# Optimization experiments

Measured on AMD Instinct MI355X. Metric: run time of the kernel, lower is better.

## Reference

```python
import jax, jax.numpy as jnp
import numpy as np

B, C, H, W = 4, 512, 128, 128
CQK = C // 8


def setup_inputs() -> dict:
    key = jax.random.key(0)
    ks = jax.random.split(key, 4)
    def w(k, shape, fan_in):
        return jax.random.normal(k, shape, jnp.float32) * np.float32(1.0 / np.sqrt(fan_in))
    return {
        "x": jax.random.normal(ks[0], (B, C, H, W), jnp.float32),
        "Wq": w(ks[1], (CQK, C), C), "bq": jnp.zeros((CQK,), jnp.float32),
        "Wk": w(ks[2], (CQK, C), C), "bk": jnp.zeros((CQK,), jnp.float32),
        "Wv": w(ks[3], (C, C), C), "bv": jnp.zeros((C,), jnp.float32),
    }


def _criss_cross(q, k, v):
    # q,k: [B, Cqk, H, W]; v: [B, C, H, W]
    _, _, h, w = q.shape
    # row energies: query at (y,x) vs keys (y, i) for all i -> [B, W(i), H, W]
    e_row = jnp.einsum('bchw,bchi->bihw', q, k)
    # column energies incl. self: query at (y,x) vs keys (j, x) -> [B, H(j), H, W]
    e_col = jnp.einsum('bchw,bcjw->bjhw', q, k)
    # CCNet's ca_weight excludes j == y from the column part (self term is
    # already counted once in the row part at i == x). Mask it to -inf so the
    # softmax matches the [B, H+W-1, H, W] energy exactly (masked weight = 0).
    diag = jnp.eye(h, dtype=bool)[None, :, :, None]  # [1, H(j), H(y), 1]
    e_col = jnp.where(diag, -jnp.inf, e_col)
    attn = jax.nn.softmax(jnp.concatenate([e_row, e_col], axis=1), axis=1)
    a_row, a_col = attn[:, :w], attn[:, w:]
    # ca_map: aggregate values along the same row and same column
    out = (jnp.einsum('bihw,bchi->bchw', a_row, v)
           + jnp.einsum('bjhw,bcjw->bchw', a_col, v))
    return out


def reference(x, Wq, bq, Wk, bk, Wv, bv):
    # 1x1 convs == per-pixel channel matmuls
    proj = lambda Wm, bm: jnp.einsum('bchw,oc->bohw', x, Wm) + bm[None, :, None, None]
    q = proj(Wq, bq)
    k = proj(Wk, bk)
    v = proj(Wv, bv)
    return _criss_cross(q, k, v)
```

## Files before the change

kernel.cpp:

```cpp
#include <hip/hip_runtime.h>
#include <hip/hip_bf16.h>

namespace {
constexpr int kB = 4;
constexpr int kC = 512;
constexpr int kH = 128;
constexpr int kW = 128;
constexpr int kCQK = 64;
constexpr int kL = kH * kW;
constexpr int kO = 640;

constexpr size_t OFF_WALL = 0;
constexpr size_t OFF_BALL = (size_t)kO * kC;
constexpr size_t OFF_QKV  = OFF_BALL + kO;
constexpr size_t OFF_E    = OFF_QKV + (size_t)kB * kO * kL;
constexpr size_t WS_FLOATS = OFF_E + (size_t)kB * kH * kW * 256;

typedef __attribute__((ext_vector_type(8))) short bf16x8;
typedef __attribute__((ext_vector_type(4))) float f32x4;

__device__ __forceinline__ unsigned short f32_to_bf16_rn(float f) {
  unsigned u = __float_as_uint(f);
  unsigned r = (u + 0x7FFFu + ((u >> 16) & 1u)) >> 16;
  return (unsigned short)r;
}
__device__ __forceinline__ float bf16_to_f32(unsigned short h) {
  return __uint_as_float(((unsigned)h) << 16);
}
__device__ __forceinline__ unsigned pack_bf16x2(float a, float b) {
  return (unsigned)f32_to_bf16_rn(a) | ((unsigned)f32_to_bf16_rn(b) << 16);
}
constexpr int SOW = 17;
constexpr int SOC = 16 * SOW + 1;
constexpr int ROW_SW = 132;
constexpr size_t AROWT_OFF = 2097152;
constexpr size_t QH_OFF = 0;
constexpr size_t QL_OFF = 1048576;
constexpr size_t KH_OFF = 2097152;
constexpr size_t KL_OFF = 3145728;
constexpr size_t CTMP_OFF = 8388608;
constexpr int VT_SC = 68;
constexpr int VT_SW = 16 * VT_SC + 4;
constexpr size_t VFRAG_B = (size_t)kW * 32 * 4 * 64 * 8;
}

__global__ __launch_bounds__(256) void pack_w(
    const float* __restrict__ Wq, const float* __restrict__ bq,
    const float* __restrict__ Wk, const float* __restrict__ bk,
    const float* __restrict__ Wv, const float* __restrict__ bv,
    short* __restrict__ wpk, float* __restrict__ ball) {
  const int r = blockIdx.x;
  const int t = threadIdx.x;
  const float* src;
  if (r < 64) {
    src = Wq + (size_t)r * kC;
    if (t == 0) ball[r] = bq[r];
  } else if (r < 128) {
    src = Wk + (size_t)(r - 64) * kC;
    if (t == 0) ball[r] = bk[r - 64];
  } else {
    src = Wv + (size_t)(r - 128) * kC;
    if (t == 0) ball[r] = bv[r - 128];
  }
#pragma unroll
  for (int p = 0; p < 2; ++p) {
    const int c = p * 256 + t;
    const float v = src[c];
    const unsigned short h = f32_to_bf16_rn(v);
    const unsigned short l = f32_to_bf16_rn(v - bf16_to_f32(h));
    wpk[(size_t)r * kC + c] = (short)h;
    wpk[(size_t)kO * kC + (size_t)r * kC + c] = (short)l;
  }
}

__global__ __launch_bounds__(256) void pack_x(
    const float* __restrict__ x, short* __restrict__ xpk, int b) {
  __shared__ float sT[64][65];
  const int l0 = blockIdx.x * 64;
  const int c0 = blockIdx.y * 64;
  const int t = threadIdx.x;
  const float* xb = x + (size_t)b * kC * kL;
#pragma unroll
  for (int p = 0; p < 4; ++p) {
    const int ch = p * 256 + t;
    const int c = ch >> 4, l4 = (ch & 15) * 4;
    float4 v = *(const float4*)(xb + (size_t)(c0 + c) * kL + l0 + l4);
    sT[c][l4 + 0] = v.x; sT[c][l4 + 1] = v.y; sT[c][l4 + 2] = v.z; sT[c][l4 + 3] = v.w;
  }
  __syncthreads();
#pragma unroll
  for (int p = 0; p < 2; ++p) {
    const int ch = p * 256 + t;
    const int l = ch >> 3, cg = ch & 7;
    short hi[8], lo[8];
#pragma unroll
    for (int j = 0; j < 8; ++j) {
      const float v = sT[cg * 8 + j][l];
      const unsigned short h = f32_to_bf16_rn(v);
      hi[j] = (short)h;
      lo[j] = (short)f32_to_bf16_rn(v - bf16_to_f32(h));
    }
    short* dh = xpk + (size_t)(l0 + l) * kC + c0 + cg * 8;
    *(bf16x8*)dh = *(bf16x8*)hi;
    *(bf16x8*)(dh + (size_t)kL * kC) = *(bf16x8*)lo;
  }
}

__global__ __launch_bounds__(256, 2) void proj_mfma(
    const short* __restrict__ xpk, const short* __restrict__ wpk,
    const float* __restrict__ ball, float* __restrict__ qkv, int b) {
  __shared__ short A_h[128 * 64];
  __shared__ short A_l[128 * 64];
  __shared__ short B_h[128 * 64];
  __shared__ short B_l[128 * 64];
  const int mt = blockIdx.x;
  const int n0 = blockIdx.y * 128;
  const int m0 = mt * 128;
  const bool qk = (mt == 0);
  const int t = threadIdx.x;
  const int wid = t >> 6, lane = t & 63;
  const int wr = wid >> 1, wc = wid & 1;
  const int lr = lane & 15, lg = lane >> 4;
  const int srow8 = lane >> 3;
  const int skg = (lane & 7) ^ srow8;

  f32x4 acc[4][4];
#pragma unroll
  for (int i = 0; i < 4; ++i)
#pragma unroll
    for (int j = 0; j < 4; ++j) acc[i][j] = (f32x4)(0.f);

  for (int kt = 0; kt < 8; ++kt) {
    const int k0 = kt * 64;
#pragma unroll
    for (int p = 0; p < 4; ++p) {
      const int ck = p * 4 + wid;
      const int row = ck * 8 + srow8;
      const short* srcA = wpk + (size_t)(m0 + row) * kC + k0 + skg * 8;
      const short* srcB = xpk + (size_t)(n0 + row) * kC + k0 + skg * 8;
      __builtin_amdgcn_global_load_lds(
          (const __attribute__((address_space(1))) void*)srcA,
          (__attribute__((address_space(3))) void*)&A_h[ck * 512], 16, 0, 0);
      __builtin_amdgcn_global_load_lds(
          (const __attribute__((address_space(1))) void*)(srcA + (size_t)kO * kC),
          (__attribute__((address_space(3))) void*)&A_l[ck * 512], 16, 0, 0);
      __builtin_amdgcn_global_load_lds(
          (const __attribute__((address_space(1))) void*)srcB,
          (__attribute__((address_space(3))) void*)&B_h[ck * 512], 16, 0, 0);
      if (qk)
        __builtin_amdgcn_global_load_lds(
            (const __attribute__((address_space(1))) void*)(srcB + (size_t)kL * kC),
            (__attribute__((address_space(3))) void*)&B_l[ck * 512], 16, 0, 0);
    }
    __syncthreads();
#pragma unroll
    for (int ks = 0; ks < 2; ++ks) {
      bf16x8 ah[4], al[4], bh[4], bl[4];
#pragma unroll
      for (int mf = 0; mf < 4; ++mf) {
        const int row = wr * 64 + mf * 16 + lr;
        const int kg = ks * 4 + lg;
        const int off = row * 64 + ((kg ^ (row & 7)) << 3);
        ah[mf] = *(const bf16x8*)&A_h[off];
        al[mf] = *(const bf16x8*)&A_l[off];
      }
#pragma unroll
      for (int nf = 0; nf < 4; ++nf) {
        const int row = wc * 64 + nf * 16 + lr;
        const int kg = ks * 4 + lg;
        const int off = row * 64 + ((kg ^ (row & 7)) << 3);
        bh[nf] = *(const bf16x8*)&B_h[off];
        if (qk) bl[nf] = *(const bf16x8*)&B_l[off];
      }
#pragma unroll
      for (int mf = 0; mf < 4; ++mf)
#pragma unroll
        for (int nf = 0; nf < 4; ++nf) {
          acc[mf][nf] = __builtin_amdgcn_mfma_f32_16x16x32_bf16(
              ah[mf], bh[nf], acc[mf][nf], 0, 0, 0);
          acc[mf][nf] = __builtin_amdgcn_mfma_f32_16x16x32_bf16(
              al[mf], bh[nf], acc[mf][nf], 0, 0, 0);
          if (qk)
            acc[mf][nf] = __builtin_amdgcn_mfma_f32_16x16x32_bf16(
                ah[mf], bl[nf], acc[mf][nf], 0, 0, 0);
        }
    }
    __syncthreads();
  }
  if (qk) {
    unsigned short* qw = (unsigned short*)qkv + (size_t)b * kO * kL * 2
        + (wr ? KH_OFF : QH_OFF);
#pragma unroll
    for (int mf = 0; mf < 4; ++mf) {
      const int c0 = mf * 16 + lg * 4;
#pragma unroll
      for (int nf = 0; nf < 4; ++nf) {
        const int l = n0 + wc * 64 + nf * 16 + lr;
        unsigned short hi4[4], lo4[4];
#pragma unroll
        for (int r = 0; r < 4; ++r) {
          const float val = acc[mf][nf][r] + ball[wr * 64 + c0 + r];
          const unsigned short h = f32_to_bf16_rn(val);
          hi4[r] = h;
          lo4[r] = f32_to_bf16_rn(val - bf16_to_f32(h));
        }
        unsigned short* d = qw + ((size_t)l * 64 + c0);
        *(uint2*)d = *(uint2*)hi4;
        *(uint2*)(d + QL_OFF) = *(uint2*)lo4;
      }
    }
  } else {
    unsigned short* vbf =
        (unsigned short*)(qkv + ((size_t)b * kO + 128) * kL);
#pragma unroll
    for (int mf = 0; mf < 4; ++mf) {
#pragma unroll
      for (int r = 0; r < 4; ++r) {
        const int m = m0 + wr * 64 + mf * 16 + lg * 4 + r;
        const float bias = ball[m];
        unsigned short* dst = vbf + (size_t)(m - 128) * kL + n0 + wc * 64;
#pragma unroll
        for (int nf = 0; nf < 4; ++nf) {
          dst[nf * 16 + lr] = f32_to_bf16_rn(acc[mf][nf][r] + bias);
        }
      }
    }
  }
}

template <int COL>
__global__ __launch_bounds__(256) void escore_mfma(
    const float* qkv, float* __restrict__ e) {
  const int bi = blockIdx.x;
  const int b = bi >> 7, idx = bi & 127;
  const int t = threadIdx.x;
  const int wid = t >> 6, lane = t & 63;
  const int wj = wid >> 1, wh = wid & 1;
  const int lr = lane & 15, lg = lane >> 4;

  const unsigned short* qkb = (const unsigned short*)qkv + (size_t)b * kO * kL * 2;
  const size_t baseoff = COL ? (size_t)idx * 64 : (size_t)idx * 8192;
  const int rstride = COL ? 8192 : 64;

  f32x4 acc[4][4];
#pragma unroll
  for (int i = 0; i < 4; ++i)
#pragma unroll
    for (int j = 0; j < 4; ++j) acc[i][j] = (f32x4)(0.f);

#pragma unroll
  for (int ks = 0; ks < 2; ++ks) {
    bf16x8 ah[4], al[4], bh[4], bl[4];
#pragma unroll
    for (int mf = 0; mf < 4; ++mf) {
      const size_t ro = baseoff + (size_t)(wj * 64 + mf * 16 + lr) * rstride
          + ks * 32 + lg * 8;
      ah[mf] = *(const bf16x8*)(qkb + KH_OFF + ro);
      al[mf] = *(const bf16x8*)(qkb + KL_OFF + ro);
    }
#pragma unroll
    for (int nf = 0; nf < 4; ++nf) {
      const size_t ro = baseoff + (size_t)(wh * 64 + nf * 16 + lr) * rstride
          + ks * 32 + lg * 8;
      bh[nf] = *(const bf16x8*)(qkb + QH_OFF + ro);
      bl[nf] = *(const bf16x8*)(qkb + QL_OFF + ro);
    }
#pragma unroll
    for (int mf = 0; mf < 4; ++mf)
#pragma unroll
      for (int nf = 0; nf < 4; ++nf) {
        acc[mf][nf] = __builtin_amdgcn_mfma_f32_16x16x32_bf16(
            ah[mf], bh[nf], acc[mf][nf], 0, 0, 0);
        acc[mf][nf] = __builtin_amdgcn_mfma_f32_16x16x32_bf16(
            ah[mf], bl[nf], acc[mf][nf], 0, 0, 0);
        acc[mf][nf] = __builtin_amdgcn_mfma_f32_16x16x32_bf16(
            al[mf], bh[nf], acc[mf][nf], 0, 0, 0);
      }
  }
  const float NEG_INF = __int_as_float(0xff800000);
#pragma unroll
  for (int mf = 0; mf < 4; ++mf) {
    const int row0 = wj * 64 + mf * 16 + lg * 4;
#pragma unroll
    for (int nf = 0; nf < 4; ++nf) {
      const int cl = wh * 64 + nf * 16 + lr;
      float o[4];
#pragma unroll
      for (int r = 0; r < 4; ++r) {
        float v = acc[mf][nf][r];
        if (COL && (row0 + r == cl)) v = NEG_INF;
        o[r] = v;
      }
      float* dst;
      if (COL)
        dst = e + (((size_t)b * kH + cl) * kW + idx) * 256 + 128 + row0;
      else
        dst = e + (((size_t)b * kH + idx) * kW + cl) * 256 + row0;
      *(float4*)dst = *(const float4*)o;
    }
  }
}

__global__ __launch_bounds__(256) void softmax_kernel(
    float* __restrict__ e, float* qkv_base) {
  const int t = threadIdx.x;
  const int wv = t >> 6, lane = t & 63;
  const size_t pix = (size_t)blockIdx.x * 4 + wv;
  float* p = e + pix * 256 + lane * 4;
  float4 v = *(const float4*)p;
  float m = fmaxf(fmaxf(v.x, v.y), fmaxf(v.z, v.w));
#pragma unroll
  for (int off = 32; off > 0; off >>= 1) m = fmaxf(m, __shfl_xor(m, off, 64));
  float e0 = expf(v.x - m), e1 = expf(v.y - m), e2 = expf(v.z - m), e3 = expf(v.w - m);
  float s = e0 + e1 + e2 + e3;
#pragma unroll
  for (int off = 32; off > 0; off >>= 1) s += __shfl_xor(s, off, 64);
  const float inv = 1.0f / s;
  const float o0 = e0 * inv, o1 = e1 * inv, o2 = e2 * inv, o3 = e3 * inv;
  const int b = (int)(pix >> 14);
  const int h = (int)((pix >> 7) & 127);
  const int w = (int)(pix & 127);
  unsigned short* base = (unsigned short*)qkv_base + (size_t)b * kO * kL * 2;
  if (lane < 32) {
    unsigned short* dst = base + AROWT_OFF + (((size_t)h * kW + w) * 128 + lane * 4);
    *(uint2*)dst = make_uint2(pack_bf16x2(o0, o1), pack_bf16x2(o2, o3));
  } else {
    const int s32 = lane - 32;
    const int jb = s32 >> 3;
    const int lg = (s32 >> 1) & 3;
    const int eoff = (s32 & 1) * 4;
    const int hb = h >> 4, hr = h & 15;
    unsigned short* dst = base + (size_t)w * 16384
        + (((size_t)(jb * 8 + hb) * 64 + lg * 16 + hr) * 8 + eoff);
    *(uint2*)dst = make_uint2(pack_bf16x2(o0, o1), pack_bf16x2(o2, o3));
  }
}

__global__ __launch_bounds__(256) void vtrans_kernel(
    const float* __restrict__ qkv, unsigned short* __restrict__ vfrag) {
  __shared__ float sT[16 * VT_SW];
  const int cb = blockIdx.x;
  const int wt = blockIdx.y;
  const int b  = blockIdx.z;
  const int t = threadIdx.x;
  const int lane = t & 63, wd = t >> 6;
  const int lr = lane & 15, lg = lane >> 4;
  const unsigned short* vb =
      (const unsigned short*)(qkv + ((size_t)b * kO + 128) * kL)
      + (size_t)(cb * 16) * kL + wt * 16;
  unsigned short* vfb = vfrag + (size_t)b * VFRAG_B;

  for (int half = 0; half < 2; ++half) {
    const int j0 = half * 64;
#pragma unroll
    for (int p = 0; p < 16; ++p) {
      const int g = p * 256 + t;
      const int wq = g & 3;
      const int j = (g >> 2) & 63;
      const int ci = p;
      uint2 v2 = *(const uint2*)(vb + (size_t)ci * kL + (size_t)(j0 + j) * kW + wq * 4);
      float* d = sT + ci * VT_SC + j;
      d[(wq * 4 + 0) * VT_SW] = bf16_to_f32((unsigned short)(v2.x & 0xffff));
      d[(wq * 4 + 1) * VT_SW] = bf16_to_f32((unsigned short)(v2.x >> 16));
      d[(wq * 4 + 2) * VT_SW] = bf16_to_f32((unsigned short)(v2.y & 0xffff));
      d[(wq * 4 + 3) * VT_SW] = bf16_to_f32((unsigned short)(v2.y >> 16));
    }
    __syncthreads();
#pragma unroll
    for (int wi = 0; wi < 4; ++wi) {
      const int w = wd * 4 + wi;
#pragma unroll
      for (int ktl = 0; ktl < 2; ++ktl) {
        const float* s = sT + w * VT_SW + lr * VT_SC + ktl * 32 + lg * 8;
        float a[8];
        *(float4*)(a + 0) = *(const float4*)(s + 0);
        *(float4*)(a + 4) = *(const float4*)(s + 4);
        const int ktg = half * 2 + ktl;
        unsigned short* dst = vfb
            + ((((size_t)(wt * 16 + w) * 32 + cb) * 4 + ktg) * 64 + lane) * 8;
        uint4 o = make_uint4(pack_bf16x2(a[0], a[1]), pack_bf16x2(a[2], a[3]),
                             pack_bf16x2(a[4], a[5]), pack_bf16x2(a[6], a[7]));
        *(uint4*)dst = o;
      }
    }
    __syncthreads();
  }
}

__global__ __launch_bounds__(1024) void colagg_mfma(
    float* qkv, const unsigned short* __restrict__ vfrag) {
  __shared__ float sO[64 * SOC];
  const int gx = blockIdx.x;
  const int ct = gx & 7, ht = gx >> 3;
  const int c0 = ct * 64, h0 = ht * 64;
  const int w0 = blockIdx.y * 16;
  const int b = blockIdx.z;
  const int t = threadIdx.x;
  const int wv = t >> 6, lane = t & 63;
  const int lr = lane & 15, lg = lane >> 4;
  const int w = w0 + wv;

  f32x4 acc[4][4];
#pragma unroll
  for (int i = 0; i < 4; ++i)
#pragma unroll
    for (int j = 0; j < 4; ++j) acc[i][j] = (f32x4)(0.f);

  const unsigned short* ab = (const unsigned short*)qkv + (size_t)b * kO * kL * 2
      + (size_t)w * 16384;
  const unsigned short* vfb = vfrag + (size_t)b * VFRAG_B
      + ((size_t)w * 32 + ct * 4) * 2048;
  unsigned short* ctmp =
      (unsigned short*)(qkv + ((size_t)b * kO + 128) * kL) + CTMP_OFF;

  for (int kt = 0; kt < 4; ++kt) {
    bf16x8 vf[4], af[4];
#pragma unroll
    for (int mf = 0; mf < 4; ++mf)
      vf[mf] = *(const bf16x8*)(vfb + ((size_t)mf * 2048 + kt * 512 + lane * 8));
#pragma unroll
    for (int nf = 0; nf < 4; ++nf)
      af[nf] = *(const bf16x8*)(
          ab + (((size_t)(kt * 8 + ht * 4 + nf) * 64 + lane) * 8));
#pragma unroll
    for (int mf = 0; mf < 4; ++mf)
#pragma unroll
      for (int nf = 0; nf < 4; ++nf)
        acc[mf][nf] = __builtin_amdgcn_mfma_f32_16x16x32_bf16(
            vf[mf], af[nf], acc[mf][nf], 0, 0, 0);
  }

  const int ew4 = t & 3, ehh = (t >> 2) & 15, ecb = t >> 6;
  for (int nf = 0; nf < 4; ++nf) {
    __syncthreads();
#pragma unroll
    for (int mf = 0; mf < 4; ++mf)
#pragma unroll
      for (int r = 0; r < 4; ++r)
        sO[(mf * 16 + lg * 4 + r) * SOC + lr * SOW + wv] = acc[mf][nf][r];
    __syncthreads();
#pragma unroll
    for (int q = 0; q < 4; ++q) {
      const int c = q * 16 + ecb;
      const float* s = &sO[c * SOC + ehh * SOW + ew4 * 4];
      unsigned u0 = pack_bf16x2(s[0], s[1]);
      unsigned u1 = pack_bf16x2(s[2], s[3]);
      unsigned short* dst = ctmp + ((size_t)(c0 + c) * kL
          + (size_t)(h0 + nf * 16 + ehh) * kW + w0 + ew4 * 4);
      *(uint2*)dst = make_uint2(u0, u1);
    }
  }
}

__global__ __launch_bounds__(256) void rowagg_mfma(
    const float* qkv, float* __restrict__ out) {
  __shared__ float sO[64 * ROW_SW];
  const int ct = blockIdx.x;
  const int bh = blockIdx.y;
  const int b = bh >> 7, h = bh & 127;
  const int c0 = ct * 128;
  const int t = threadIdx.x;
  const int wid = t >> 6, lane = t & 63;
  const int wr = wid >> 1, wc = wid & 1;
  const int lr = lane & 15, lg = lane >> 4;

  f32x4 acc[4][4];
#pragma unroll
  for (int i = 0; i < 4; ++i)
#pragma unroll
    for (int j = 0; j < 4; ++j) acc[i][j] = (f32x4)(0.f);

  const unsigned short* vbf =
      (const unsigned short*)(qkv + ((size_t)b * kO + 128) * kL);
  const unsigned short* ctmp = vbf + CTMP_OFF;
  const unsigned short* arbase = (const unsigned short*)qkv
      + (size_t)b * kO * kL * 2 + AROWT_OFF + (size_t)h * kW * 128;

#pragma unroll
  for (int s = 0; s < 4; ++s) {
    bf16x8 vfr[4], afr[4];
#pragma unroll
    for (int mf = 0; mf < 4; ++mf) {
      const int c = c0 + wr * 64 + mf * 16 + lr;
      vfr[mf] = *(const bf16x8*)(
          vbf + (size_t)c * kL + (size_t)h * kW + s * 32 + lg * 8);
    }
#pragma unroll
    for (int nf = 0; nf < 4; ++nf) {
      const int w = wc * 64 + nf * 16 + lr;
      afr[nf] = *(const bf16x8*)(arbase + (size_t)w * 128 + s * 32 + lg * 8);
    }
#pragma unroll
    for (int mf = 0; mf < 4; ++mf)
#pragma unroll
      for (int nf = 0; nf < 4; ++nf)
        acc[mf][nf] = __builtin_amdgcn_mfma_f32_16x16x32_bf16(
            vfr[mf], afr[nf], acc[mf][nf], 0, 0, 0);
  }

  const int wq = t & 31;
  const int cc8 = t >> 5;
  const unsigned short* ctb = ctmp + (size_t)h * kW;
  float* outb = out + ((size_t)b * kC * kL + (size_t)h * kW);
  for (int half = 0; half < 2; ++half) {
    if (wr == half) {
#pragma unroll
      for (int mf = 0; mf < 4; ++mf)
#pragma unroll
        for (int nf = 0; nf < 4; ++nf)
#pragma unroll
          for (int r = 0; r < 4; ++r)
            sO[(mf * 16 + lg * 4 + r) * ROW_SW + wc * 64 + nf * 16 + lr] =
                acc[mf][nf][r];
    }
    __syncthreads();
#pragma unroll
    for (int i = 0; i < 8; ++i) {
      const int cl = i * 8 + cc8;
      const size_t c = c0 + half * 64 + cl;
      float4 v = *(const float4*)&sO[cl * ROW_SW + wq * 4];
      uint2 c2 = *(const uint2*)(ctb + c * kL + wq * 4);
      v.x += bf16_to_f32((unsigned short)(c2.x & 0xffff));
      v.y += bf16_to_f32((unsigned short)(c2.x >> 16));
      v.z += bf16_to_f32((unsigned short)(c2.y & 0xffff));
      v.w += bf16_to_f32((unsigned short)(c2.y >> 16));
      *(float4*)(outb + c * kL + wq * 4) = v;
    }
    __syncthreads();
  }
}

extern "C" void kernel_launch(void* const* d_in, const int* in_sizes, int n_in,
                              void* d_out, int out_size, void* d_ws, size_t ws_size,
                              hipStream_t stream) {
  (void)in_sizes; (void)n_in; (void)out_size; (void)ws_size;
  const float* x  = (const float*)d_in[0];
  const float* Wq = (const float*)d_in[1];
  const float* bq = (const float*)d_in[2];
  const float* Wk = (const float*)d_in[3];
  const float* bk = (const float*)d_in[4];
  const float* Wv = (const float*)d_in[5];
  const float* bv = (const float*)d_in[6];
  float* out = (float*)d_out;
  float* ws  = (float*)d_ws;

  short* wpk = (short*)(ws + OFF_WALL);
  float* ball = ws + OFF_BALL;
  float* qkv  = ws + OFF_QKV;
  float* e    = ws + OFF_E;
  short* xpk  = (short*)(ws + OFF_E);
  unsigned short* vfrag = (unsigned short*)(ws + OFF_E);

  pack_w<<<dim3(kO), dim3(256), 0, stream>>>(Wq, bq, Wk, bk, Wv, bv, wpk, ball);
  for (int b = 0; b < kB; ++b) {
    pack_x<<<dim3(kL / 64, kC / 64), dim3(256), 0, stream>>>(x, xpk, b);
    proj_mfma<<<dim3(5, kL / 128), dim3(256), 0, stream>>>(xpk, wpk, ball, qkv, b);
  }
  escore_mfma<0><<<dim3(kB * kH), dim3(256), 0, stream>>>(qkv, e);
  escore_mfma<1><<<dim3(kB * kW), dim3(256), 0, stream>>>(qkv, e);
  softmax_kernel<<<dim3(kB * kH * kW / 4), dim3(256), 0, stream>>>(e, qkv);
  vtrans_kernel<<<dim3(32, 8, kB), dim3(256), 0, stream>>>(qkv, vfrag);
  colagg_mfma<<<dim3(16, kW / 16, kB), dim3(1024), 0, stream>>>(qkv, vfrag);
  rowagg_mfma<<<dim3(4, kB * kH), dim3(256), 0, stream>>>(qkv, out);
}
```

Baseline: 415.9 us.

## Batch projection launches and write transposed Q/K copy for column scores

When the workspace is large enough, all batches are packed and projected in single launches using a per-batch xpk buffer, rather than a loop of per-batch launches. The projection epilogue also writes a column-major (w,h) copy of the Q/K hi/lo fragments into a scratch region. The column-score kernel can then read contiguous 64-channel rows instead of striding by 8192 elements. This costs extra workspace and extra global writes in the projection step.

```diff
diff --git a/kernel.cpp b/kernel.cpp
--- a/kernel.cpp
+++ b/kernel.cpp
@@ -74,12 +74,15 @@
 }
 
 __global__ __launch_bounds__(256) void pack_x(
-    const float* __restrict__ x, short* __restrict__ xpk, int b) {
+    const float* __restrict__ x, short* __restrict__ xpk,
+    int b_off, size_t xstride) {
   __shared__ float sT[64][65];
   const int l0 = blockIdx.x * 64;
   const int c0 = blockIdx.y * 64;
+  const int b = b_off + blockIdx.z;
   const int t = threadIdx.x;
   const float* xb = x + (size_t)b * kC * kL;
+  short* xo = xpk + (size_t)blockIdx.z * xstride;
 #pragma unroll
   for (int p = 0; p < 4; ++p) {
     const int ch = p * 256 + t;
@@ -100,15 +103,16 @@
       hi[j] = (short)h;
       lo[j] = (short)f32_to_bf16_rn(v - bf16_to_f32(h));
     }
-    short* dh = xpk + (size_t)(l0 + l) * kC + c0 + cg * 8;
+    short* dh = xo + (size_t)(l0 + l) * kC + c0 + cg * 8;
     *(bf16x8*)dh = *(bf16x8*)hi;
     *(bf16x8*)(dh + (size_t)kL * kC) = *(bf16x8*)lo;
   }
 }
 
 __global__ __launch_bounds__(256, 2) void proj_mfma(
-    const short* __restrict__ xpk, const short* __restrict__ wpk,
-    const float* __restrict__ ball, float* __restrict__ qkv, int b) {
+    const short* __restrict__ xpk, size_t xstride,
+    const short* __restrict__ wpk,
+    const float* __restrict__ ball, float* __restrict__ qkv, int b_off) {
   __shared__ short A_h[128 * 64];
   __shared__ short A_l[128 * 64];
   __shared__ short B_h[128 * 64];
@@ -116,6 +120,7 @@
   const int mt = blockIdx.x;
   const int n0 = blockIdx.y * 128;
   const int m0 = mt * 128;
+  const int b = b_off + blockIdx.z;
   const bool qk = (mt == 0);
   const int t = threadIdx.x;
   const int wid = t >> 6, lane = t & 63;
@@ -123,6 +128,7 @@
   const int lr = lane & 15, lg = lane >> 4;
   const int srow8 = lane >> 3;
   const int skg = (lane & 7) ^ srow8;
+  const short* xo = xpk + (size_t)blockIdx.z * xstride;
 
   f32x4 acc[4][4];
 #pragma unroll
@@ -137,7 +143,7 @@
       const int ck = p * 4 + wid;
       const int row = ck * 8 + srow8;
       const short* srcA = wpk + (size_t)(m0 + row) * kC + k0 + skg * 8;
-      const short* srcB = xpk + (size_t)(n0 + row) * kC + k0 + skg * 8;
+      const short* srcB = xo + (size_t)(n0 + row) * kC + k0 + skg * 8;
       __builtin_amdgcn_global_load_lds(
           (const __attribute__((address_space(1))) void*)srcA,
           (__attribute__((address_space(3))) void*)&A_h[ck * 512], 16, 0, 0);
@@ -190,6 +196,8 @@
   if (qk) {
     unsigned short* qw = (unsigned short*)qkv + (size_t)b * kO * kL * 2
         + (wr ? KH_OFF : QH_OFF);
+    unsigned short* tb = (unsigned short*)(qkv + ((size_t)b * kO + 128) * kL)
+        + CTMP_OFF + (wr ? 2097152 : 0);
 #pragma unroll
     for (int mf = 0; mf < 4; ++mf) {
       const int c0 = mf * 16 + lg * 4;
@@ -207,6 +215,10 @@
         unsigned short* d = qw + ((size_t)l * 64 + c0);
         *(uint2*)d = *(uint2*)hi4;
         *(uint2*)(d + QL_OFF) = *(uint2*)lo4;
+        const int hh = l >> 7, ww = l & 127;
+        unsigned short* dT = tb + (((size_t)ww * 128 + hh) * 64 + c0);
+        *(uint2*)dT = *(uint2*)hi4;
+        *(uint2*)(dT + 1048576) = *(uint2*)lo4;
       }
     }
   } else {
@@ -230,7 +242,9 @@
 
 template <int COL>
 __global__ __launch_bounds__(256) void escore_mfma(
-    const float* qkv, float* __restrict__ e) {
+    const unsigned short* __restrict__ qh, const unsigned short* __restrict__ ql,
+    const unsigned short* __restrict__ kh, const unsigned short* __restrict__ kl,
+    float* __restrict__ e) {
   const int bi = blockIdx.x;
   const int b = bi >> 7, idx = bi & 127;
   const int t = threadIdx.x;
@@ -238,9 +252,7 @@
   const int wj = wid >> 1, wh = wid & 1;
   const int lr = lane & 15, lg = lane >> 4;
 
-  const unsigned short* qkb = (const unsigned short*)qkv + (size_t)b * kO * kL * 2;
-  const size_t baseoff = COL ? (size_t)idx * 64 : (size_t)idx * 8192;
-  const int rstride = COL ? 8192 : 64;
+  const size_t base = (size_t)b * ((size_t)kO * kL * 2) + (size_t)idx * 8192;
 
   f32x4 acc[4][4];
 #pragma unroll
@@ -253,17 +265,17 @@
     bf16x8 ah[4], al[4], bh[4], bl[4];
 #pragma unroll
     for (int mf = 0; mf < 4; ++mf) {
-      const size_t ro = baseoff + (size_t)(wj * 64 + mf * 16 + lr) * rstride
+      const size_t ro = base + (size_t)(wj * 64 + mf * 16 + lr) * 64
           + ks * 32 + lg * 8;
-      ah[mf] = *(const bf16x8*)(qkb + KH_OFF + ro);
-      al[mf] = *(const bf16x8*)(qkb + KL_OFF + ro);
+      ah[mf] = *(const bf16x8*)(kh + ro);
+      al[mf] = *(const bf16x8*)(kl + ro);
     }
 #pragma unroll
     for (int nf = 0; nf < 4; ++nf) {
-      const size_t ro = baseoff + (size_t)(wh * 64 + nf * 16 + lr) * rstride
+      const size_t ro = base + (size_t)(wh * 64 + nf * 16 + lr) * 64
           + ks * 32 + lg * 8;
-      bh[nf] = *(const bf16x8*)(qkb + QH_OFF + ro);
-      bl[nf] = *(const bf16x8*)(qkb + QL_OFF + ro);
+      bh[nf] = *(const bf16x8*)(qh + ro);
+      bl[nf] = *(const bf16x8*)(ql + ro);
     }
 #pragma unroll
     for (int mf = 0; mf < 4; ++mf)
@@ -533,7 +545,7 @@
 extern "C" void kernel_launch(void* const* d_in, const int* in_sizes, int n_in,
                               void* d_out, int out_size, void* d_ws, size_t ws_size,
                               hipStream_t stream) {
-  (void)in_sizes; (void)n_in; (void)out_size; (void)ws_size;
+  (void)in_sizes; (void)n_in; (void)out_size;
   const float* x  = (const float*)d_in[0];
   const float* Wq = (const float*)d_in[1];
   const float* bq = (const float*)d_in[2];
@@ -548,16 +560,34 @@
   float* ball = ws + OFF_BALL;
   float* qkv  = ws + OFF_QKV;
   float* e    = ws + OFF_E;
-  short* xpk  = (short*)(ws + OFF_E);
   unsigned short* vfrag = (unsigned short*)(ws + OFF_E);
 
   pack_w<<<dim3(kO), dim3(256), 0, stream>>>(Wq, bq, Wk, bk, Wv, bv, wpk, ball);
-  for (int b = 0; b < kB; ++b) {
-    pack_x<<<dim3(kL / 64, kC / 64), dim3(256), 0, stream>>>(x, xpk, b);
-    proj_mfma<<<dim3(5, kL / 128), dim3(256), 0, stream>>>(xpk, wpk, ball, qkv, b);
-  }
-  escore_mfma<0><<<dim3(kB * kH), dim3(256), 0, stream>>>(qkv, e);
-  escore_mfma<1><<<dim3(kB * kW), dim3(256), 0, stream>>>(qkv, e);
+
+  const size_t xpk_batch = (size_t)2 * kL * kC;
+  const size_t need = WS_FLOATS * sizeof(float)
+      + (size_t)kB * xpk_batch * sizeof(short);
+  if (ws_size >= need) {
+    short* xall = (short*)(ws + WS_FLOATS);
+    pack_x<<<dim3(kL / 64, kC / 64, kB), dim3(256), 0, stream>>>(
+        x, xall, 0, xpk_batch);
+    proj_mfma<<<dim3(5, kL / 128, kB), dim3(256), 0, stream>>>(
+        xall, xpk_batch, wpk, ball, qkv, 0);
+  } else {
+    short* xpk = (short*)(ws + OFF_E);
+    for (int b = 0; b < kB; ++b) {
+      pack_x<<<dim3(kL / 64, kC / 64, 1), dim3(256), 0, stream>>>(x, xpk, b, 0);
+      proj_mfma<<<dim3(5, kL / 128, 1), dim3(256), 0, stream>>>(
+          xpk, 0, wpk, ball, qkv, b);
+    }
+  }
+
+  unsigned short* qkb0 = (unsigned short*)qkv;
+  escore_mfma<0><<<dim3(kB * kH), dim3(256), 0, stream>>>(
+      qkb0 + QH_OFF, qkb0 + QL_OFF, qkb0 + KH_OFF, qkb0 + KL_OFF, e);
+  unsigned short* vt0 = (unsigned short*)qkv + (size_t)128 * kL * 2 + CTMP_OFF;
+  escore_mfma<1><<<dim3(kB * kW), dim3(256), 0, stream>>>(
+      vt0 + 0, vt0 + 1048576, vt0 + 2097152, vt0 + 3145728, e);
   softmax_kernel<<<dim3(kB * kH * kW / 4), dim3(256), 0, stream>>>(e, qkv);
   vtrans_kernel<<<dim3(32, 8, kB), dim3(256), 0, stream>>>(qkv, vfrag);
   colagg_mfma<<<dim3(16, kW / 16, kB), dim3(1024), 0, stream>>>(qkv, vfrag);
```

Measured after the change: 397.9 us. 4.3% less time.
